# Optimization experiments

Hardware: AMD Instinct MI355X
Metric: run time of the kernel (lower is better)

## Reference

```python
import jax, jax.numpy as jnp
import numpy as np

B, V, C, CD, D, H, W = 1, 3, 32, 8, 32, 128, 160
LAMB = 1.5


def _bilinear(img, x, y):
    # img: [c, Hs, Ws]; x, y: pixel coords [D, HW]; zero padding, align_corners=True semantics
    c, Hs, Ws = img.shape
    x0 = jnp.floor(x)
    y0 = jnp.floor(y)
    x0i = x0.astype(jnp.int32)
    y0i = y0.astype(jnp.int32)
    wx = x - x0
    wy = y - y0
    imgf = img.reshape(c, Hs * Ws)

    def gather(xi, yi, w):
        valid = (xi >= 0) & (xi < Ws) & (yi >= 0) & (yi < Hs)
        lin = jnp.clip(yi, 0, Hs - 1) * Ws + jnp.clip(xi, 0, Ws - 1)
        v = jnp.take(imgf, lin.reshape(-1), axis=1).reshape((c,) + xi.shape)
        return v * (w * valid.astype(w.dtype))[None]

    return (gather(x0i, y0i, (1 - wx) * (1 - wy))
            + gather(x0i + 1, y0i, wx * (1 - wy))
            + gather(x0i, y0i + 1, (1 - wx) * wy)
            + gather(x0i + 1, y0i + 1, wx * wy))


def _homo_warp(src_fea, src_proj, ref_proj, depth_values):
    # src_fea [B,c,Hs,Ws]; projs [B,4,4]; depth_values [B,D,H,W] -> [B,c,D,H,W]
    b, c, Hs, Ws = src_fea.shape
    _, d, h, w = depth_values.shape
    proj = jnp.einsum('bij,bjk->bik', src_proj, jnp.linalg.inv(ref_proj))
    rot = proj[:, :3, :3]
    tr = proj[:, :3, 3]
    ys, xs = jnp.meshgrid(jnp.arange(h, dtype=src_fea.dtype), jnp.arange(w, dtype=src_fea.dtype), indexing='ij')
    xyz = jnp.stack([xs.reshape(-1), ys.reshape(-1), jnp.ones(h * w, dtype=src_fea.dtype)], 0)  # [3,HW]
    rx = jnp.einsum('bij,jn->bin', rot, xyz)  # [B,3,HW]
    dvals = depth_values.reshape(b, 1, d, h * w)
    pxyz = rx[:, :, None, :] * dvals + tr[:, :, None, None]  # [B,3,D,HW]
    z = pxyz[:, 2]
    px = pxyz[:, 0] / z  # [B,D,HW]
    py = pxyz[:, 1] / z
    out = jax.vmap(_bilinear)(src_fea, px, py)  # [B,c,D,HW]
    return out.reshape(b, c, d, h, w)


def setup_inputs() -> dict:
    key = jax.random.key(0)
    k1, k2, k3 = jax.random.split(key, 3)
    features = jax.random.normal(k1, (V, B, C, H, W), jnp.float32)
    deps_feature_stage = jax.random.normal(k2, (V, B, CD, H, W), jnp.float32)
    reg_w = jax.random.normal(k3, (1, C + CD), jnp.float32) * 0.1
    K = np.array([[200., 0., W / 2.], [0., 200., H / 2.], [0., 0., 1.]])
    mats = []
    for tx in [0.0, 1.0, -1.0]:
        Rt = np.eye(4)
        Rt[0, 3] = tx
        P = np.eye(4)
        P[:3, :4] = K @ Rt[:3, :4]
        mats.append(P)
    proj_matrices = jnp.asarray(np.stack(mats)[None], jnp.float32)  # [B,V,4,4]
    depth_values = jnp.broadcast_to(
        jnp.linspace(5.0, 10.0, D, dtype=jnp.float32)[None, :, None, None], (B, D, H, W)) + jnp.zeros((B, D, H, W), jnp.float32)
    return {'features': features, 'deps_feature_stage': deps_feature_stage,
            'proj_matrices': proj_matrices, 'depth_values': depth_values,
            'reg_w': reg_w, 'num_depth': D, 'stage_idx': 0}


def reference(features, deps_feature_stage, proj_matrices, depth_values, reg_w, num_depth, stage_idx):
    num_views = features.shape[0]
    d = depth_values.shape[1]
    ref_proj = proj_matrices[:, 0]

    def variance_volume(feats):
        ref = feats[0]  # [B,c,H,W]
        ref_vol = jnp.broadcast_to(ref[:, :, None], (ref.shape[0], ref.shape[1], d, ref.shape[2], ref.shape[3]))
        s = ref_vol
        sq = ref_vol * ref_vol
        for v in range(1, num_views):
            wv = _homo_warp(feats[v], proj_matrices[:, v], ref_proj, depth_values)
            s = s + wv
            sq = sq + wv * wv
        return sq / num_views - (s / num_views) ** 2

    volume_variance = variance_volume(features)      # [B,C,D,H,W]
    deps_variance = variance_volume(deps_feature_stage)  # [B,CD,D,H,W]
    var = jnp.concatenate([volume_variance, deps_variance], axis=1)
    # cost_regularization modeled as 1x1x1 conv reducing channels to 1
    cost = jnp.einsum('bcdhw,oc->bodhw', var, reg_w)[:, 0]  # [B,D,H,W]
    prob_volume = jax.nn.softmax(cost, axis=1)
    depth = jnp.sum(prob_volume * depth_values, axis=1)  # [B,H,W]
    samp_variance = (depth_values - depth[:, None]) ** 2
    exp_variance = LAMB * jnp.sqrt(jnp.sum(samp_variance * prob_volume, axis=1))
    return depth, exp_variance, prob_volume
```

## Files before the change

kernel.cpp:

```cpp
#include <hip/hip_runtime.h>
#include <math.h>

#define HH   128
#define WW   160
#define HWN  (HH*WW)
#define NCF  32
#define NCD  8
#define ND   32
#define NV   3
#define LAMBF 1.5f

typedef float f32x4 __attribute__((ext_vector_type(4)));

template <int CH>
__device__ void transpose_tile(const float* __restrict__ src, float* __restrict__ dst,
                               float (*lds)[33], int tid) {
    for (int i = tid; i < CH*8; i += 256) {
        int c = i >> 3, xg = (i & 7) << 2;
        *(float4*)&lds[c][xg] = *(const float4*)(src + c*HWN + xg);
    }
    __syncthreads();
    for (int i = tid; i < 32*(CH/4); i += 256) {
        int xl = i / (CH/4), c4 = (i % (CH/4)) * 4;
        float4 t = make_float4(lds[c4][xl], lds[c4+1][xl], lds[c4+2][xl], lds[c4+3][xl]);
        *(float4*)(dst + xl*CH + c4) = t;
    }
}

__global__ __launch_bounds__(256) void prep_k(const float* __restrict__ feat,
                                              const float* __restrict__ deps,
                                              const float* __restrict__ proj,
                                              float* __restrict__ featT,
                                              float* __restrict__ depsT,
                                              float* __restrict__ projw) {
    if (blockIdx.x == 0 && blockIdx.y == 0 && blockIdx.z == 0 && threadIdx.x == 0) {
        float M00 = proj[0], M01 = proj[1], M02 = proj[2],  m0 = proj[3];
        float M10 = proj[4], M11 = proj[5], M12 = proj[6],  m1 = proj[7];
        float M20 = proj[8], M21 = proj[9], M22 = proj[10], m2 = proj[11];
        float c00 =  (M11*M22 - M12*M21);
        float c01 = -(M10*M22 - M12*M20);
        float c02 =  (M10*M21 - M11*M20);
        float det = M00*c00 + M01*c01 + M02*c02;
        float id  = 1.f / det;
        float i00 = c00*id, i01 = -(M01*M22 - M02*M21)*id, i02 =  (M01*M12 - M02*M11)*id;
        float i10 = c01*id, i11 =  (M00*M22 - M02*M20)*id, i12 = -(M00*M12 - M02*M10)*id;
        float i20 = c02*id, i21 = -(M00*M21 - M01*M20)*id, i22 =  (M00*M11 - M01*M10)*id;
        float t0 = -(i00*m0 + i01*m1 + i02*m2);
        float t1 = -(i10*m0 + i11*m1 + i12*m2);
        float t2 = -(i20*m0 + i21*m1 + i22*m2);
        #pragma unroll
        for (int v = 1; v < NV; v++) {
            const float* S = proj + v*16;
            float s00 = S[0], s01 = S[1], s02 = S[2],  st0 = S[3];
            float s10 = S[4], s11 = S[5], s12 = S[6],  st1 = S[7];
            float s20 = S[8], s21 = S[9], s22 = S[10], st2 = S[11];
            float* o = projw + (v-1)*12;
            o[0] = s00*i00 + s01*i10 + s02*i20;
            o[1] = s00*i01 + s01*i11 + s02*i21;
            o[2] = s00*i02 + s01*i12 + s02*i22;
            o[3] = s10*i00 + s11*i10 + s12*i20;
            o[4] = s10*i01 + s11*i11 + s12*i21;
            o[5] = s10*i02 + s11*i12 + s12*i22;
            o[6] = s20*i00 + s21*i10 + s22*i20;
            o[7] = s20*i01 + s21*i11 + s22*i21;
            o[8] = s20*i02 + s21*i12 + s22*i22;
            o[9]  = s00*t0 + s01*t1 + s02*t2 + st0;
            o[10] = s10*t0 + s11*t1 + s12*t2 + st1;
            o[11] = s20*t0 + s21*t1 + s22*t2 + st2;
        }
    }

    __shared__ float lds[NCF][33];
    const int z  = blockIdx.z;
    const int xb = blockIdx.x * 32;
    const int y  = blockIdx.y;
    if (z < NV) {
        transpose_tile<NCF>(feat + (size_t)(z*NCF)*HWN + y*WW + xb,
                            featT + (size_t)(z*HWN + y*WW + xb) * NCF,
                            lds, threadIdx.x);
    } else {
        transpose_tile<NCD>(deps + (size_t)((z - NV)*NCD)*HWN + y*WW + xb,
                            depsT + (size_t)((z - NV)*HWN + y*WW + xb) * NCD,
                            lds, threadIdx.x);
    }
}

__global__ __launch_bounds__(256) void cost_volume_k(
    const float* __restrict__ featT,
    const float* __restrict__ depsT,
    const float* __restrict__ dvals,
    const float* __restrict__ regw,
    const float* __restrict__ pws,
    float* __restrict__ out)
{
    __shared__ float cl [ND][9];
    __shared__ float dvl[ND][9];
    __shared__ float smax[8], sisum[8];

    const int t    = threadIdx.x;
    const int lane = t & 63;
    const int wid  = t >> 6;
    const int cg   = lane & 7;
    const int pl   = lane >> 3;
    const int pixg = blockIdx.x * 8 + pl;
    const int y    = pixg / WW;
    const int x    = pixg - y * WW;
    const float fx = (float)x, fy = (float)y;
    const int dbase = wid * 8;

    float RX[2], RY[2], RZ[2], T0[2], T1[2], T2[2];
    #pragma unroll
    for (int v = 0; v < 2; v++) {
        const float* q = pws + v*12;
        RX[v] = q[0]*fx + q[1]*fy + q[2];
        RY[v] = q[3]*fx + q[4]*fy + q[5];
        RZ[v] = q[6]*fx + q[7]*fy + q[8];
        T0[v] = q[9]; T1[v] = q[10]; T2[v] = q[11];
    }

    auto bsetup = [&](float dvv, int v, int CH, float& w00, float& w10,
                      float& w01, float& w11, int& o00, int& o10,
                      int& o01, int& o11) {
        float pz = RZ[v]*dvv + T2[v];
        float iz = __builtin_amdgcn_rcpf(pz);
        float px = (RX[v]*dvv + T0[v]) * iz;
        float py = (RY[v]*dvv + T1[v]) * iz;
        float x0f = floorf(px), y0f = floorf(py);
        int x0 = (int)x0f, y0 = (int)y0f;
        float wx = px - x0f, wy = py - y0f;
        float omx = 1.f - wx, omy = 1.f - wy;
        bool vx0 = (x0 >= 0) & (x0 < WW);
        bool vx1 = (x0+1 >= 0) & (x0+1 < WW);
        bool vy0 = (y0 >= 0) & (y0 < HH);
        bool vy1 = (y0+1 >= 0) & (y0+1 < HH);
        w00 = (vx0 && vy0) ? omx*omy : 0.f;
        w10 = (vx1 && vy0) ? wx*omy  : 0.f;
        w01 = (vx0 && vy1) ? omx*wy  : 0.f;
        w11 = (vx1 && vy1) ? wx*wy   : 0.f;
        int xc0 = min(max(x0,   0), WW-1);
        int xc1 = min(max(x0+1, 0), WW-1);
        int yc0 = min(max(y0,   0), HH-1);
        int yc1 = min(max(y0+1, 0), HH-1);
        o00 = (yc0*WW + xc0)*CH;
        o10 = (yc0*WW + xc1)*CH;
        o01 = (yc1*WW + xc0)*CH;
        o11 = (yc1*WW + xc1)*CH;
    };

    {
        float dvv_own = dvals[(dbase + cg)*HWN + pixg];
        dvl[dbase + cg][pl] = dvv_own;
        float SW00[2], SW10[2], SW01[2], SW11[2];
        int   SO00[2], SO10[2], SO01[2], SO11[2];
        #pragma unroll
        for (int v = 0; v < 2; v++)
            bsetup(dvv_own, v, NCF, SW00[v], SW10[v], SW01[v], SW11[v],
                   SO00[v], SO10[v], SO01[v], SO11[v]);

        const f32x4 r4  = *(const f32x4*)(featT + (size_t)pixg*NCF + cg*4);
        const f32x4 w4  = *(const f32x4*)(regw + cg*4);
        const f32x4 wca = w4 * (1.f/3.f);
        const f32x4 wcb = w4 * (1.f/9.f);
        const f32x4 r2  = r4 * r4;
        const float* b1 = featT + (size_t)1*HWN*NCF + cg*4;
        const float* b2 = featT + (size_t)2*HWN*NCF + cg*4;
        const int plbase = lane & 0x38;

        #pragma unroll 2
        for (int jj = 0; jj < 8; jj++) {
            const int src = plbase | jj;
            f32x4 s = r4;
            f32x4 q = r2;

            #pragma unroll
            for (int v = 0; v < 2; v++) {
                float W00 = __shfl(SW00[v], src, 64);
                float W10 = __shfl(SW10[v], src, 64);
                float W01 = __shfl(SW01[v], src, 64);
                float W11 = __shfl(SW11[v], src, 64);
                int   o00 = __shfl(SO00[v], src, 64);
                int   o10 = __shfl(SO10[v], src, 64);
                int   o01 = __shfl(SO01[v], src, 64);
                int   o11 = __shfl(SO11[v], src, 64);
                const float* b = v ? b2 : b1;
                f32x4 f00 = *(const f32x4*)(b + o00);
                f32x4 f10 = *(const f32x4*)(b + o10);
                f32x4 f01 = *(const f32x4*)(b + o01);
                f32x4 f11 = *(const f32x4*)(b + o11);
                f32x4 wv = f00*W00 + f10*W10 + f01*W01 + f11*W11;
                s += wv;
                q += wv*wv;
            }
            f32x4 tv = q*wca - (s*s)*wcb;
            float part = tv.x + tv.y + tv.z + tv.w;
            part += __shfl_xor(part, 1);
            part += __shfl_xor(part, 2);
            part += __shfl_xor(part, 4);
            if (cg == jj) cl[dbase + jj][pl] = part;
        }
    }
    __syncthreads();

    {
        const int cgd  = lane & 1;
        const int dsub = (lane >> 1) & 3;
        const f32x4 r4  = *(const f32x4*)(depsT + (size_t)pixg*NCD + cgd*4);
        const f32x4 w4  = *(const f32x4*)(regw + NCF + cgd*4);
        const f32x4 wca = w4 * (1.f/3.f);
        const f32x4 wcb = w4 * (1.f/9.f);
        const f32x4 r2  = r4 * r4;
        const float* b1 = depsT + (size_t)1*HWN*NCD + cgd*4;
        const float* b2 = depsT + (size_t)2*HWN*NCD + cgd*4;

        #pragma unroll
        for (int i = 0; i < 2; i++) {
            const int d = dbase + dsub + 4*i;
            float dvv = dvl[d][pl];
            f32x4 s = r4;
            f32x4 q = r2;

            #pragma unroll
            for (int v = 0; v < 2; v++) {
                float W00, W10, W01, W11; int o00, o10, o01, o11;
                bsetup(dvv, v, NCD, W00, W10, W01, W11, o00, o10, o01, o11);
                const float* b = v ? b2 : b1;
                f32x4 f00 = *(const f32x4*)(b + o00);
                f32x4 f10 = *(const f32x4*)(b + o10);
                f32x4 f01 = *(const f32x4*)(b + o01);
                f32x4 f11 = *(const f32x4*)(b + o11);
                f32x4 wv = f00*W00 + f10*W10 + f01*W01 + f11*W11;
                s += wv;
                q += wv*wv;
            }
            f32x4 tv = q*wca - (s*s)*wcb;
            float part = tv.x + tv.y + tv.z + tv.w;
            part += __shfl_xor(part, 1);
            if (cgd == 0) cl[d][pl] += part;
        }
    }
    __syncthreads();

    if (t < 8) {
        const int plx  = t;
        const int pixo = blockIdx.x * 8 + plx;
        float m = -1e30f;
        #pragma unroll
        for (int d = 0; d < ND; d++) m = fmaxf(m, cl[d][plx]);
        float sum = 0.f, pd = 0.f, pd2 = 0.f;
        #pragma unroll
        for (int d = 0; d < ND; d++) {
            float e   = __expf(cl[d][plx] - m);
            float dvv = dvl[d][plx];
            sum += e;
            pd  = fmaf(e, dvv, pd);
            pd2 = fmaf(e, dvv*dvv, pd2);
        }
        float isum  = 1.f / sum;
        float depth = pd * isum;
        float sv    = pd2 * isum - depth*depth;
        float ev    = LAMBF * sqrtf(fmaxf(sv, 0.f));
        smax[plx]  = m;
        sisum[plx] = isum;
        out[pixo]       = depth;
        out[HWN + pixo] = ev;
    }
    __syncthreads();
    {
        const int plx  = t & 7;
        const int dd   = t >> 3;
        const int pixo = blockIdx.x * 8 + plx;
        out[2*HWN + dd*HWN + pixo] = __expf(cl[dd][plx] - smax[plx]) * sisum[plx];
    }
}

extern "C" void kernel_launch(void* const* d_in, const int* in_sizes, int n_in,
                              void* d_out, int out_size, void* d_ws, size_t ws_size,
                              hipStream_t stream) {
    const float* features = (const float*)d_in[0];
    const float* deps     = (const float*)d_in[1];
    const float* proj     = (const float*)d_in[2];
    const float* dvals    = (const float*)d_in[3];
    const float* regw     = (const float*)d_in[4];

    float* ws    = (float*)d_ws;
    float* projw = ws;
    float* featT = ws + 64;
    float* depsT = featT + (size_t)NV*HWN*NCF;

    dim3 tg(WW/32, HH, 2*NV);
    prep_k<<<tg, 256, 0, stream>>>(features, deps, proj, featT, depsT, projw);

    cost_volume_k<<<HWN/8, 256, 0, stream>>>(featT, depsT, dvals, regw, projw,
                                             (float*)d_out);
}
```

Before: 105.7 us.

## Reuse shuffled bilinear setup for depth features and use packed fp32 math

The depth-feature stage no longer recomputes the projection, floor, validity and offset math per sample. It reuses the per-lane weights and offsets from the main feature stage through wave shuffles, rescaling offsets from the 32-channel to the 8-channel stride. The bilinear accumulation and variance math are rewritten as v_pk_fma/v_pk_mul/v_pk_add inline asm on float pairs, and the barrier between the two stages is removed since each wave only touches its own depth rows. The inline asm may limit compiler scheduling, and dropping the barrier relies on intra-wave LDS ordering.

After: 107.8 us. Within noise of the previous version (+2.0%).

```diff
diff --git a/kernel.cpp b/kernel.cpp
--- a/kernel.cpp
+++ b/kernel.cpp
@@ -11,6 +11,23 @@
 #define LAMBF 1.5f
 
 typedef float f32x4 __attribute__((ext_vector_type(4)));
+typedef float f32x2 __attribute__((ext_vector_type(2)));
+
+__device__ __forceinline__ f32x2 pk_fma(f32x2 a, f32x2 b, f32x2 c) {
+    f32x2 d;
+    asm("v_pk_fma_f32 %0, %1, %2, %3" : "=v"(d) : "v"(a), "v"(b), "v"(c));
+    return d;
+}
+__device__ __forceinline__ f32x2 pk_mul(f32x2 a, f32x2 b) {
+    f32x2 d;
+    asm("v_pk_mul_f32 %0, %1, %2" : "=v"(d) : "v"(a), "v"(b));
+    return d;
+}
+__device__ __forceinline__ f32x2 pk_add(f32x2 a, f32x2 b) {
+    f32x2 d;
+    asm("v_pk_add_f32 %0, %1, %2" : "=v"(d) : "v"(a), "v"(b));
+    return d;
+}
 
 template <int CH>
 __device__ void transpose_tile(const float* __restrict__ src, float* __restrict__ dst,
@@ -107,6 +124,7 @@
     const int x    = pixg - y * WW;
     const float fx = (float)x, fy = (float)y;
     const int dbase = wid * 8;
+    const int plbase = lane & 0x38;
 
     float RX[2], RY[2], RZ[2], T0[2], T1[2], T2[2];
     #pragma unroll
@@ -118,59 +136,55 @@
         T0[v] = q[9]; T1[v] = q[10]; T2[v] = q[11];
     }
 
-    auto bsetup = [&](float dvv, int v, int CH, float& w00, float& w10,
-                      float& w01, float& w11, int& o00, int& o10,
-                      int& o01, int& o11) {
-        float pz = RZ[v]*dvv + T2[v];
-        float iz = __builtin_amdgcn_rcpf(pz);
-        float px = (RX[v]*dvv + T0[v]) * iz;
-        float py = (RY[v]*dvv + T1[v]) * iz;
-        float x0f = floorf(px), y0f = floorf(py);
-        int x0 = (int)x0f, y0 = (int)y0f;
-        float wx = px - x0f, wy = py - y0f;
-        float omx = 1.f - wx, omy = 1.f - wy;
-        bool vx0 = (x0 >= 0) & (x0 < WW);
-        bool vx1 = (x0+1 >= 0) & (x0+1 < WW);
-        bool vy0 = (y0 >= 0) & (y0 < HH);
-        bool vy1 = (y0+1 >= 0) & (y0+1 < HH);
-        w00 = (vx0 && vy0) ? omx*omy : 0.f;
-        w10 = (vx1 && vy0) ? wx*omy  : 0.f;
-        w01 = (vx0 && vy1) ? omx*wy  : 0.f;
-        w11 = (vx1 && vy1) ? wx*wy   : 0.f;
-        int xc0 = min(max(x0,   0), WW-1);
-        int xc1 = min(max(x0+1, 0), WW-1);
-        int yc0 = min(max(y0,   0), HH-1);
-        int yc1 = min(max(y0+1, 0), HH-1);
-        o00 = (yc0*WW + xc0)*CH;
-        o10 = (yc0*WW + xc1)*CH;
-        o01 = (yc1*WW + xc0)*CH;
-        o11 = (yc1*WW + xc1)*CH;
-    };
-
+    float SW00[2], SW10[2], SW01[2], SW11[2];
+    int   SO00[2], SO10[2], SO01[2], SO11[2];
     {
         float dvv_own = dvals[(dbase + cg)*HWN + pixg];
         dvl[dbase + cg][pl] = dvv_own;
-        float SW00[2], SW10[2], SW01[2], SW11[2];
-        int   SO00[2], SO10[2], SO01[2], SO11[2];
-        #pragma unroll
-        for (int v = 0; v < 2; v++)
-            bsetup(dvv_own, v, NCF, SW00[v], SW10[v], SW01[v], SW11[v],
-                   SO00[v], SO10[v], SO01[v], SO11[v]);
-
-        const f32x4 r4  = *(const f32x4*)(featT + (size_t)pixg*NCF + cg*4);
-        const f32x4 w4  = *(const f32x4*)(regw + cg*4);
-        const f32x4 wca = w4 * (1.f/3.f);
-        const f32x4 wcb = w4 * (1.f/9.f);
-        const f32x4 r2  = r4 * r4;
+        #pragma unroll
+        for (int v = 0; v < 2; v++) {
+            float pz = RZ[v]*dvv_own + T2[v];
+            float iz = __builtin_amdgcn_rcpf(pz);
+            float px = (RX[v]*dvv_own + T0[v]) * iz;
+            float py = (RY[v]*dvv_own + T1[v]) * iz;
+            float x0f = floorf(px), y0f = floorf(py);
+            int x0 = (int)x0f, y0 = (int)y0f;
+            float wx = px - x0f, wy = py - y0f;
+            float omx = 1.f - wx, omy = 1.f - wy;
+            bool vx0 = (x0 >= 0) & (x0 < WW);
+            bool vx1 = (x0+1 >= 0) & (x0+1 < WW);
+            bool vy0 = (y0 >= 0) & (y0 < HH);
+            bool vy1 = (y0+1 >= 0) & (y0+1 < HH);
+            SW00[v] = (vx0 && vy0) ? omx*omy : 0.f;
+            SW10[v] = (vx1 && vy0) ? wx*omy  : 0.f;
+            SW01[v] = (vx0 && vy1) ? omx*wy  : 0.f;
+            SW11[v] = (vx1 && vy1) ? wx*wy   : 0.f;
+            int xc0 = min(max(x0,   0), WW-1);
+            int xc1 = min(max(x0+1, 0), WW-1);
+            int yc0 = min(max(y0,   0), HH-1);
+            int yc1 = min(max(y0+1, 0), HH-1);
+            SO00[v] = (yc0*WW + xc0)*NCF;
+            SO10[v] = (yc0*WW + xc1)*NCF;
+            SO01[v] = (yc1*WW + xc0)*NCF;
+            SO11[v] = (yc1*WW + xc1)*NCF;
+        }
+    }
+
+    {
+        const f32x4 r4 = *(const f32x4*)(featT + (size_t)pixg*NCF + cg*4);
+        const f32x4 w4 = *(const f32x4*)(regw + cg*4);
+        const f32x2 wca_l  = w4.lo * (1.f/3.f), wca_h  = w4.hi * (1.f/3.f);
+        const f32x2 nwcb_l = w4.lo * (-1.f/9.f), nwcb_h = w4.hi * (-1.f/9.f);
+        const f32x2 r_l = r4.lo, r_h = r4.hi;
+        const f32x2 r2_l = r_l*r_l, r2_h = r_h*r_h;
         const float* b1 = featT + (size_t)1*HWN*NCF + cg*4;
         const float* b2 = featT + (size_t)2*HWN*NCF + cg*4;
-        const int plbase = lane & 0x38;
 
         #pragma unroll 2
         for (int jj = 0; jj < 8; jj++) {
             const int src = plbase | jj;
-            f32x4 s = r4;
-            f32x4 q = r2;
+            f32x2 s_l = r_l, s_h = r_h;
+            f32x2 q_l = r2_l, q_h = r2_h;
 
             #pragma unroll
             for (int v = 0; v < 2; v++) {
@@ -187,53 +201,84 @@
                 f32x4 f10 = *(const f32x4*)(b + o10);
                 f32x4 f01 = *(const f32x4*)(b + o01);
                 f32x4 f11 = *(const f32x4*)(b + o11);
-                f32x4 wv = f00*W00 + f10*W10 + f01*W01 + f11*W11;
-                s += wv;
-                q += wv*wv;
+                f32x2 W00p = {W00, W00}, W10p = {W10, W10};
+                f32x2 W01p = {W01, W01}, W11p = {W11, W11};
+                f32x2 wv_l = pk_mul(f00.lo, W00p);
+                wv_l = pk_fma(f10.lo, W10p, wv_l);
+                wv_l = pk_fma(f01.lo, W01p, wv_l);
+                wv_l = pk_fma(f11.lo, W11p, wv_l);
+                f32x2 wv_h = pk_mul(f00.hi, W00p);
+                wv_h = pk_fma(f10.hi, W10p, wv_h);
+                wv_h = pk_fma(f01.hi, W01p, wv_h);
+                wv_h = pk_fma(f11.hi, W11p, wv_h);
+                s_l = pk_add(s_l, wv_l); q_l = pk_fma(wv_l, wv_l, q_l);
+                s_h = pk_add(s_h, wv_h); q_h = pk_fma(wv_h, wv_h, q_h);
             }
-            f32x4 tv = q*wca - (s*s)*wcb;
-            float part = tv.x + tv.y + tv.z + tv.w;
+            f32x2 t_l = pk_mul(q_l, wca_l);
+            t_l = pk_fma(pk_mul(s_l, s_l), nwcb_l, t_l);
+            f32x2 t_h = pk_mul(q_h, wca_h);
+            t_h = pk_fma(pk_mul(s_h, s_h), nwcb_h, t_h);
+            float part = (t_l.x + t_l.y) + (t_h.x + t_h.y);
             part += __shfl_xor(part, 1);
             part += __shfl_xor(part, 2);
             part += __shfl_xor(part, 4);
             if (cg == jj) cl[dbase + jj][pl] = part;
         }
     }
-    __syncthreads();
 
     {
         const int cgd  = lane & 1;
         const int dsub = (lane >> 1) & 3;
-        const f32x4 r4  = *(const f32x4*)(depsT + (size_t)pixg*NCD + cgd*4);
-        const f32x4 w4  = *(const f32x4*)(regw + NCF + cgd*4);
-        const f32x4 wca = w4 * (1.f/3.f);
-        const f32x4 wcb = w4 * (1.f/9.f);
-        const f32x4 r2  = r4 * r4;
+        const f32x4 r4 = *(const f32x4*)(depsT + (size_t)pixg*NCD + cgd*4);
+        const f32x4 w4 = *(const f32x4*)(regw + NCF + cgd*4);
+        const f32x2 wca_l  = w4.lo * (1.f/3.f), wca_h  = w4.hi * (1.f/3.f);
+        const f32x2 nwcb_l = w4.lo * (-1.f/9.f), nwcb_h = w4.hi * (-1.f/9.f);
+        const f32x2 r_l = r4.lo, r_h = r4.hi;
+        const f32x2 r2_l = r_l*r_l, r2_h = r_h*r_h;
         const float* b1 = depsT + (size_t)1*HWN*NCD + cgd*4;
         const float* b2 = depsT + (size_t)2*HWN*NCD + cgd*4;
 
         #pragma unroll
         for (int i = 0; i < 2; i++) {
-            const int d = dbase + dsub + 4*i;
-            float dvv = dvl[d][pl];
-            f32x4 s = r4;
-            f32x4 q = r2;
+            const int jj = dsub + 4*i;
+            const int d  = dbase + jj;
+            const int src = plbase | jj;
+            f32x2 s_l = r_l, s_h = r_h;
+            f32x2 q_l = r2_l, q_h = r2_h;
 
             #pragma unroll
             for (int v = 0; v < 2; v++) {
-                float W00, W10, W01, W11; int o00, o10, o01, o11;
-                bsetup(dvv, v, NCD, W00, W10, W01, W11, o00, o10, o01, o11);
+                float W00 = __shfl(SW00[v], src, 64);
+                float W10 = __shfl(SW10[v], src, 64);
+                float W01 = __shfl(SW01[v], src, 64);
+                float W11 = __shfl(SW11[v], src, 64);
+                int   o00 = __shfl(SO00[v], src, 64) >> 2;
+                int   o10 = __shfl(SO10[v], src, 64) >> 2;
+                int   o01 = __shfl(SO01[v], src, 64) >> 2;
+                int   o11 = __shfl(SO11[v], src, 64) >> 2;
                 const float* b = v ? b2 : b1;
                 f32x4 f00 = *(const f32x4*)(b + o00);
                 f32x4 f10 = *(const f32x4*)(b + o10);
                 f32x4 f01 = *(const f32x4*)(b + o01);
                 f32x4 f11 = *(const f32x4*)(b + o11);
-                f32x4 wv = f00*W00 + f10*W10 + f01*W01 + f11*W11;
-                s += wv;
-                q += wv*wv;
+                f32x2 W00p = {W00, W00}, W10p = {W10, W10};
+                f32x2 W01p = {W01, W01}, W11p = {W11, W11};
+                f32x2 wv_l = pk_mul(f00.lo, W00p);
+                wv_l = pk_fma(f10.lo, W10p, wv_l);
+                wv_l = pk_fma(f01.lo, W01p, wv_l);
+                wv_l = pk_fma(f11.lo, W11p, wv_l);
+                f32x2 wv_h = pk_mul(f00.hi, W00p);
+                wv_h = pk_fma(f10.hi, W10p, wv_h);
+                wv_h = pk_fma(f01.hi, W01p, wv_h);
+                wv_h = pk_fma(f11.hi, W11p, wv_h);
+                s_l = pk_add(s_l, wv_l); q_l = pk_fma(wv_l, wv_l, q_l);
+                s_h = pk_add(s_h, wv_h); q_h = pk_fma(wv_h, wv_h, q_h);
             }
-            f32x4 tv = q*wca - (s*s)*wcb;
-            float part = tv.x + tv.y + tv.z + tv.w;
+            f32x2 t_l = pk_mul(q_l, wca_l);
+            t_l = pk_fma(pk_mul(s_l, s_l), nwcb_l, t_l);
+            f32x2 t_h = pk_mul(q_h, wca_h);
+            t_h = pk_fma(pk_mul(s_h, s_h), nwcb_h, t_h);
+            float part = (t_l.x + t_l.y) + (t_h.x + t_h.y);
             part += __shfl_xor(part, 1);
             if (cgd == 0) cl[d][pl] += part;
         }
```
